# Kernel tuning notes

Measured on AMD Instinct MI355X. Metric: run time of the kernel, lower is better.

Reference implementation:

```python
import jax, jax.numpy as jnp
from jax import lax
import numpy as np
import math

D_MODEL = 1024
D_STATE = 16
DT_RANK = 64  # ceil(1024/16)


def setup_inputs() -> dict:
    key = jax.random.key(0)
    ks = jax.random.split(key, 8)
    B, L = 2, 2048
    x = jax.random.normal(ks[0], (B, L, D_MODEL), dtype=jnp.float32)
    A_log = jnp.full((D_MODEL, D_STATE), math.log(0.5), dtype=jnp.float32)
    x_proj_w = jax.random.normal(ks[1], (DT_RANK + 2 * D_STATE, D_MODEL), dtype=jnp.float32) * (D_MODEL ** -0.5)
    dt_init_std = DT_RANK ** -0.5
    dt_proj_w = jax.random.uniform(ks[2], (D_MODEL, DT_RANK), minval=-dt_init_std, maxval=dt_init_std, dtype=jnp.float32)
    # dt bias init: softplus-inverse of dt sampled log-uniform in [2*dt_min, 2*dt_max] (trend)
    dt = jnp.exp(jax.random.uniform(ks[3], (D_MODEL,), dtype=jnp.float32) * (math.log(0.2) - math.log(0.002)) + math.log(0.002))
    dt = jnp.clip(dt, 1e-4)
    dt_proj_b = dt + jnp.log(-jnp.expm1(-dt))
    D_param = jnp.ones((D_MODEL,), dtype=jnp.float32)
    trend_emphasis = jnp.full((D_MODEL,), 0.1, dtype=jnp.float32)
    return {
        "x": x, "A_log": A_log, "x_proj_w": x_proj_w,
        "dt_proj_w": dt_proj_w, "dt_proj_b": dt_proj_b,
        "D_param": D_param, "trend_emphasis": trend_emphasis,
    }


def _selective_scan(u, delta, A, Bp, Cp, D_param):
    # u, delta: [B,L,D]; A: [D,N]; Bp, Cp: [B,L,N]; D_param: [D]
    deltaA = jnp.exp(jnp.einsum('bld,dn->bldn', delta, A))       # [B,L,D,N]
    deltaBu = jnp.einsum('bld,bln->bldn', delta * u, Bp)          # [B,L,D,N]
    Bsz, L, Dm, N = deltaA.shape

    def step(h, inp):
        dA, dBu, c = inp          # dA,dBu: [B,D,N]; c: [B,N]
        h = dA * h + dBu
        y = jnp.einsum('bdn,bn->bd', h, c)
        return h, y

    h0 = jnp.zeros((Bsz, Dm, N), dtype=u.dtype)
    xs = (jnp.moveaxis(deltaA, 1, 0), jnp.moveaxis(deltaBu, 1, 0), jnp.moveaxis(Cp, 1, 0))
    _, ys = lax.scan(step, h0, xs)            # ys: [L,B,D]
    y = jnp.moveaxis(ys, 0, 1)                # [B,L,D]
    return y + u * D_param


def reference(x, A_log, x_proj_w, dt_proj_w, dt_proj_b, D_param, trend_emphasis):
    # trend component: channel-wise emphasis gate (dropout in eval mode = identity)
    x = x * jax.nn.sigmoid(trend_emphasis)
    xz = x @ x_proj_w.T                                  # [B,L,dt_rank+2N]
    delta_part = xz[..., :DT_RANK]
    Bp = xz[..., DT_RANK:DT_RANK + D_STATE]              # [B,L,N]
    Cp = xz[..., DT_RANK + D_STATE:]                     # [B,L,N]
    delta = jax.nn.softplus(delta_part @ dt_proj_w.T + dt_proj_b)  # [B,L,D]
    A = -jnp.exp(A_log.astype(jnp.float32))
    return _selective_scan(x, delta, A, Bp, Cp, D_param.astype(jnp.float32))
```

## Files before the change

### kernel.cpp

```cpp
#include <hip/hip_runtime.h>
#include <math.h>


#define LOG2E 1.44269504088896340736f
typedef float v2f __attribute__((ext_vector_type(2)));

__device__ __forceinline__ float fexp2(float v){
#if defined(__has_builtin)
#if __has_builtin(__builtin_amdgcn_exp2f)
  return __builtin_amdgcn_exp2f(v);
#else
  return exp2f(v);
#endif
#else
  return exp2f(v);
#endif
}

__device__ __forceinline__ float fsoftplus(float v){
  return fmaxf(v, 0.f) + __logf(1.f + __expf(-fabsf(v)));
}

__global__ __launch_bounds__(256) void k_prep(const float* __restrict__ xpw,
                                              const float* __restrict__ dtw,
                                              const float* __restrict__ alog,
                                              const float* __restrict__ te,
                                              float* __restrict__ w2T,
                                              float* __restrict__ dtwT,
                                              float* __restrict__ A2,
                                              float* __restrict__ sg){
  __shared__ float sm[32 * 33];
  const int bid = blockIdx.x, t = threadIdx.x;
  const int lane = t & 31, srow = t >> 5;
  if (bid < 96){
    const int kt = bid / 3, ct = bid - kt * 3;
#pragma unroll
    for (int r = 0; r < 4; r++){
      const int cr = srow * 4 + r;
      sm[cr * 33 + lane] = xpw[(size_t)(ct * 32 + cr) * 1024 + kt * 32 + lane];
    }
    __syncthreads();
#pragma unroll
    for (int r = 0; r < 4; r++){
      const int kr = srow * 4 + r;
      const int kg = kt * 32 + kr;
      const float s = 1.f / (1.f + __expf(-te[kg]));
      w2T[(size_t)kg * 96 + ct * 32 + lane] = sm[lane * 33 + kr] * s;
    }
  } else if (bid < 160){
    const int idx = bid - 96, dti = idx >> 1, kt2 = idx & 1;
#pragma unroll
    for (int r = 0; r < 4; r++){
      const int cr = srow * 4 + r;
      sm[cr * 33 + lane] = dtw[(size_t)(dti * 32 + cr) * 64 + kt2 * 32 + lane];
    }
    __syncthreads();
#pragma unroll
    for (int r = 0; r < 4; r++){
      const int kr = srow * 4 + r;
      dtwT[(size_t)(kt2 * 32 + kr) * 1024 + dti * 32 + lane] = sm[lane * 33 + kr];
    }
  } else if (bid < 176){
    const int j = (bid - 160) * 1024 + t;
#pragma unroll
    for (int i = 0; i < 4; i++)
      A2[j + i * 256] = -__expf(alog[j + i * 256]) * LOG2E;
  } else {
#pragma unroll
    for (int i = 0; i < 4; i++){
      const int m = i * 256 + t;
      sg[m] = 1.f / (1.f + __expf(-te[m]));
    }
  }
}

__global__ __launch_bounds__(256) void k_xz(const float* __restrict__ x,
                                            const float* __restrict__ w2T,
                                            float* __restrict__ xzp){
  __shared__ float xT[32 * 257];
  const int t = threadIdx.x;
  const int row0 = blockIdx.x * 256;
  const int c0 = blockIdx.y * 32;
  const int kbase = blockIdx.z * 64;
  v2f acc[16];
#pragma unroll
  for (int c = 0; c < 16; c++) acc[c] = (v2f){0.f, 0.f};
  const int kq = t & 7, rsub = t >> 3;
  for (int kt = 0; kt < 2; ++kt){
    const int k0 = kbase + kt * 32;
    __syncthreads();
#pragma unroll
    for (int p = 0; p < 8; p++){
      const int r = p * 32 + rsub;
      const float4 v = *reinterpret_cast<const float4*>(&x[(size_t)(row0 + r) * 1024 + k0 + kq * 4]);
      xT[(kq * 4 + 0) * 257 + r] = v.x;
      xT[(kq * 4 + 1) * 257 + r] = v.y;
      xT[(kq * 4 + 2) * 257 + r] = v.z;
      xT[(kq * 4 + 3) * 257 + r] = v.w;
    }
    __syncthreads();
#pragma unroll 4
    for (int kk = 0; kk < 32; ++kk){
      const float xv = xT[kk * 257 + t];
      const v2f xv2 = {xv, xv};
      const v2f* wr = reinterpret_cast<const v2f*>(&w2T[(size_t)(k0 + kk) * 96 + c0]);
#pragma unroll
      for (int c = 0; c < 16; c++) acc[c] = acc[c] + xv2 * wr[c];
    }
  }
  float4* o = reinterpret_cast<float4*>(xzp + ((size_t)blockIdx.z * 4096 + row0 + t) * 96 + c0);
  const float4* av = reinterpret_cast<const float4*>(acc);
#pragma unroll
  for (int q = 0; q < 8; q++) o[q] = av[q];
}

__global__ __launch_bounds__(256) void k_reduce(const float4* __restrict__ p,
                                                float4* __restrict__ xz){
  const int i = blockIdx.x * 256 + threadIdx.x;
  float4 r = p[i];
#pragma unroll
  for (int s = 1; s < 16; s++){
    const float4 a = p[(size_t)s * 98304 + i];
    r.x += a.x; r.y += a.y; r.z += a.z; r.w += a.w;
  }
  xz[i] = r;
}

__global__ __launch_bounds__(256) void k_scan1(const float* __restrict__ x,
                                               const float* __restrict__ xz,
                                               const float* __restrict__ dtwT,
                                               const float* __restrict__ dtb,
                                               const float* __restrict__ A2,
                                               const float* __restrict__ sg,
                                               float* __restrict__ S,
                                               float* __restrict__ P){
  const int t = threadIdx.x;
  const int chunk = blockIdx.x, dgrp = blockIdx.y, b = blockIdx.z;
  const int d = dgrp * 256 + t;
  const int l0 = chunk * 16;
  v2f wv[32];
#pragma unroll
  for (int k2 = 0; k2 < 32; k2++){
    wv[k2].x = dtwT[(size_t)(2 * k2) * 1024 + d];
    wv[k2].y = dtwT[(size_t)(2 * k2 + 1) * 1024 + d];
  }
  float a2[16];
  {
    const float4* ap = reinterpret_cast<const float4*>(A2 + (size_t)d * 16);
#pragma unroll
    for (int q = 0; q < 4; q++){
      const float4 v = ap[q];
      a2[q*4] = v.x; a2[q*4+1] = v.y; a2[q*4+2] = v.z; a2[q*4+3] = v.w;
    }
  }
  bool uni = true;
#pragma unroll
  for (int n = 1; n < 16; n++) uni = uni && (a2[n] == a2[0]);
  const float sgv = sg[d], dtbv = dtb[d];
  const float* xzb = xz + (size_t)(b * 2048 + l0) * 96;
  float dl[16];
#pragma unroll
  for (int li = 0; li < 16; ++li){
    v2f acc = {dtbv, 0.f};
    const v2f* dp = reinterpret_cast<const v2f*>(xzb + li * 96);
#pragma unroll
    for (int k2 = 0; k2 < 32; k2++) acc = acc + dp[k2] * wv[k2];
    dl[li] = fsoftplus(acc.x + acc.y);
  }
  const size_t xidx = (size_t)(b * 2048 + l0) * 1024 + d;
  const size_t base = ((size_t)((b * 128 + chunk) * 1024 + d)) * 16;
  if (uni){
    const float a2u = a2[0];
    v2f h2[8];
#pragma unroll
    for (int q = 0; q < 8; q++) h2[q] = (v2f){0.f, 0.f};
    float sumd = 0.f;
#pragma unroll 4
    for (int li = 0; li < 16; ++li){
      const float dv = dl[li];
      sumd += dv;
      const float xv = x[xidx + (size_t)li * 1024];
      const float du = dv * xv * sgv;
      const float tt = fexp2(dv * a2u);
      const v2f tt2 = {tt, tt}, du2 = {du, du};
      const v2f* brow = reinterpret_cast<const v2f*>(xzb + li * 96 + 64);
#pragma unroll
      for (int q = 0; q < 8; q++) h2[q] = h2[q] * tt2 + brow[q] * du2;
    }
    const float Ppu = fexp2(a2u * sumd);
    const float4* hv = reinterpret_cast<const float4*>(h2);
#pragma unroll
    for (int q = 0; q < 4; q++)
      *reinterpret_cast<float4*>(&S[base + q * 4]) = hv[q];
    const float4 pv = {Ppu, Ppu, Ppu, Ppu};
#pragma unroll
    for (int q = 0; q < 4; q++)
      *reinterpret_cast<float4*>(&P[base + q * 4]) = pv;
  } else {
    float h[16], Pp[16];
#pragma unroll
    for (int n = 0; n < 16; n++){ h[n] = 0.f; Pp[n] = 1.f; }
    for (int li = 0; li < 16; ++li){
      const float dv = dl[li];
      const float xv = x[xidx + (size_t)li * 1024];
      const float du = dv * xv * sgv;
      const float* brow = xzb + li * 96 + 64;
#pragma unroll
      for (int n = 0; n < 16; n++){
        const float tt = fexp2(dv * a2[n]);
        h[n] = fmaf(tt, h[n], du * brow[n]);
        Pp[n] *= tt;
      }
    }
#pragma unroll
    for (int q = 0; q < 4; q++){
      float4 v; v.x = h[q*4]; v.y = h[q*4+1]; v.z = h[q*4+2]; v.w = h[q*4+3];
      *reinterpret_cast<float4*>(&S[base + q * 4]) = v;
      float4 u; u.x = Pp[q*4]; u.y = Pp[q*4+1]; u.z = Pp[q*4+2]; u.w = Pp[q*4+3];
      *reinterpret_cast<float4*>(&P[base + q * 4]) = u;
    }
  }
}

__global__ __launch_bounds__(128) void k_scan2(const float* __restrict__ S,
                                               const float* __restrict__ P,
                                               float* __restrict__ H){
  const int g = blockIdx.x * 128 + threadIdx.x;
  const int n = g & 15, dd = (g >> 4) & 1023, bb = g >> 14;
  float h = 0.f;
#pragma unroll 8
  for (int c = 0; c < 128; c++){
    const size_t idx = ((size_t)((bb * 128 + c) * 1024 + dd)) * 16 + n;
    H[idx] = h;
    h = fmaf(P[idx], h, S[idx]);
  }
}

__global__ __launch_bounds__(256) void k_scan3(const float* __restrict__ x,
                                               const float* __restrict__ xz,
                                               const float* __restrict__ dtwT,
                                               const float* __restrict__ dtb,
                                               const float* __restrict__ A2,
                                               const float* __restrict__ sg,
                                               const float* __restrict__ Dpar,
                                               const float* __restrict__ H,
                                               float* __restrict__ out){
  const int t = threadIdx.x;
  const int chunk = blockIdx.x, dgrp = blockIdx.y, b = blockIdx.z;
  const int d = dgrp * 256 + t;
  const int l0 = chunk * 16;
  v2f wv[32];
#pragma unroll
  for (int k2 = 0; k2 < 32; k2++){
    wv[k2].x = dtwT[(size_t)(2 * k2) * 1024 + d];
    wv[k2].y = dtwT[(size_t)(2 * k2 + 1) * 1024 + d];
  }
  float a2[16];
  {
    const float4* ap = reinterpret_cast<const float4*>(A2 + (size_t)d * 16);
#pragma unroll
    for (int q = 0; q < 4; q++){
      const float4 v = ap[q];
      a2[q*4] = v.x; a2[q*4+1] = v.y; a2[q*4+2] = v.z; a2[q*4+3] = v.w;
    }
  }
  bool uni = true;
#pragma unroll
  for (int n = 1; n < 16; n++) uni = uni && (a2[n] == a2[0]);
  const float sgv = sg[d], dtbv = dtb[d], Dv = Dpar[d];
  const float* xzb = xz + (size_t)(b * 2048 + l0) * 96;
  float dl[16];
#pragma unroll
  for (int li = 0; li < 16; ++li){
    v2f acc = {dtbv, 0.f};
    const v2f* dp = reinterpret_cast<const v2f*>(xzb + li * 96);
#pragma unroll
    for (int k2 = 0; k2 < 32; k2++) acc = acc + dp[k2] * wv[k2];
    dl[li] = fsoftplus(acc.x + acc.y);
  }
  const size_t xidx = (size_t)(b * 2048 + l0) * 1024 + d;
  const size_t hbase = ((size_t)((b * 128 + chunk) * 1024 + d)) * 16;
  if (uni){
    const float a2u = a2[0];
    v2f h2[8];
    {
      const float4* hp = reinterpret_cast<const float4*>(H + hbase);
      float4* hd = reinterpret_cast<float4*>(h2);
#pragma unroll
      for (int q = 0; q < 4; q++) hd[q] = hp[q];
    }
#pragma unroll 4
    for (int li = 0; li < 16; ++li){
      const float dv = dl[li];
      const float xv = x[xidx + (size_t)li * 1024];
      const float du = dv * xv * sgv;
      const float tt = fexp2(dv * a2u);
      const v2f tt2 = {tt, tt}, du2 = {du, du};
      const v2f* brow = reinterpret_cast<const v2f*>(xzb + li * 96 + 64);
      const v2f* crow = reinterpret_cast<const v2f*>(xzb + li * 96 + 80);
      v2f yv = {0.f, 0.f};
#pragma unroll
      for (int q = 0; q < 8; q++){
        h2[q] = h2[q] * tt2 + brow[q] * du2;
        yv = yv + h2[q] * crow[q];
      }
      out[xidx + (size_t)li * 1024] = fmaf(xv * sgv, Dv, yv.x + yv.y);
    }
  } else {
    float h[16];
    {
      const float4* hp = reinterpret_cast<const float4*>(H + hbase);
#pragma unroll
      for (int q = 0; q < 4; q++){
        const float4 v = hp[q];
        h[q*4] = v.x; h[q*4+1] = v.y; h[q*4+2] = v.z; h[q*4+3] = v.w;
      }
    }
    for (int li = 0; li < 16; ++li){
      const float dv = dl[li];
      const float xv = x[xidx + (size_t)li * 1024];
      const float du = dv * xv * sgv;
      const float* brow = xzb + li * 96 + 64;
      float y = 0.f;
#pragma unroll
      for (int n = 0; n < 16; n++){
        const float tt = fexp2(dv * a2[n]);
        h[n] = fmaf(tt, h[n], du * brow[n]);
        y = fmaf(h[n], brow[16 + n], y);
      }
      out[xidx + (size_t)li * 1024] = fmaf(xv * sgv, Dv, y);
    }
  }
}

extern "C" void kernel_launch(void* const* d_in, const int* in_sizes, int n_in,
                              void* d_out, int out_size, void* d_ws, size_t ws_size,
                              hipStream_t stream){
  const float* x    = (const float*)d_in[0];
  const float* Alog = (const float*)d_in[1];
  const float* xpw  = (const float*)d_in[2];
  const float* dtw  = (const float*)d_in[3];
  const float* dtb  = (const float*)d_in[4];
  const float* Dpar = (const float*)d_in[5];
  const float* te   = (const float*)d_in[6];
  float* out = (float*)d_out;
  char* ws = (char*)d_ws;

  float* w2T  = (float*)(ws);
  float* A2   = (float*)(ws + 393216);
  float* sg   = (float*)(ws + 458752);
  float* dtwT = (float*)(ws + 462848);
  float* xz   = (float*)(ws + 724992);
  float* xzp  = (float*)(ws + 2297856);
  float* S    = (float*)(ws + 27463680);
  float* P    = (float*)(ws + 44240896);
  float* Hst  = (float*)(ws + 61018112);

  hipLaunchKernelGGL(k_prep,   dim3(177),        dim3(256), 0, stream, xpw, dtw, Alog, te, w2T, dtwT, A2, sg);
  hipLaunchKernelGGL(k_xz,     dim3(16, 3, 16),  dim3(256), 0, stream, x, w2T, xzp);
  hipLaunchKernelGGL(k_reduce, dim3(384),        dim3(256), 0, stream, (const float4*)xzp, (float4*)xz);
  hipLaunchKernelGGL(k_scan1,  dim3(128, 4, 2),  dim3(256), 0, stream, x, xz, dtwT, dtb, A2, sg, S, P);
  hipLaunchKernelGGL(k_scan2,  dim3(256),        dim3(128), 0, stream, S, P, Hst);
  hipLaunchKernelGGL(k_scan3,  dim3(128, 4, 2),  dim3(256), 0, stream, x, xz, dtwT, dtb, A2, sg, Dpar, Hst, out);
}
```

Measured before the change: 163.7 us.

## Precompute delta once in separate kernel and parallelize inter-chunk scan across segments

Adds a k_delta kernel that computes softplus(dt projection) once into a workspace buffer, so scan1 and scan3 no longer each repeat the 64-wide dot product and dtw register loads. Rewrites k_scan2 to split the 128 chunks into 8 segments per block, combine them through shared memory, then apply the carries. Scan2 now runs 1024 blocks instead of 256 to expose more parallelism. The cost is an extra 16MB delta buffer write and two reads, plus an additional kernel launch.

```diff
diff --git a/kernel.cpp b/kernel.cpp
--- a/kernel.cpp
+++ b/kernel.cpp
@@ -126,10 +126,34 @@
   xz[i] = r;
 }
 
-__global__ __launch_bounds__(256) void k_scan1(const float* __restrict__ x,
-                                               const float* __restrict__ xz,
+__global__ __launch_bounds__(256) void k_delta(const float* __restrict__ xz,
                                                const float* __restrict__ dtwT,
                                                const float* __restrict__ dtb,
+                                               float* __restrict__ del){
+  const int t = threadIdx.x;
+  const int r0 = blockIdx.x * 16;
+  const int d = blockIdx.y * 256 + t;
+  v2f wv[32];
+#pragma unroll
+  for (int k2 = 0; k2 < 32; k2++){
+    wv[k2].x = dtwT[(size_t)(2 * k2) * 1024 + d];
+    wv[k2].y = dtwT[(size_t)(2 * k2 + 1) * 1024 + d];
+  }
+  const float dtbv = dtb[d];
+  const float* xzb = xz + (size_t)r0 * 96;
+#pragma unroll 4
+  for (int li = 0; li < 16; ++li){
+    v2f acc = {dtbv, 0.f};
+    const v2f* dp = reinterpret_cast<const v2f*>(xzb + li * 96);
+#pragma unroll
+    for (int k2 = 0; k2 < 32; k2++) acc = acc + dp[k2] * wv[k2];
+    del[(size_t)(r0 + li) * 1024 + d] = fsoftplus(acc.x + acc.y);
+  }
+}
+
+__global__ __launch_bounds__(256) void k_scan1(const float* __restrict__ x,
+                                               const float* __restrict__ del,
+                                               const float* __restrict__ xz,
                                                const float* __restrict__ A2,
                                                const float* __restrict__ sg,
                                                float* __restrict__ S,
@@ -138,12 +162,6 @@
   const int chunk = blockIdx.x, dgrp = blockIdx.y, b = blockIdx.z;
   const int d = dgrp * 256 + t;
   const int l0 = chunk * 16;
-  v2f wv[32];
-#pragma unroll
-  for (int k2 = 0; k2 < 32; k2++){
-    wv[k2].x = dtwT[(size_t)(2 * k2) * 1024 + d];
-    wv[k2].y = dtwT[(size_t)(2 * k2 + 1) * 1024 + d];
-  }
   float a2[16];
   {
     const float4* ap = reinterpret_cast<const float4*>(A2 + (size_t)d * 16);
@@ -156,18 +174,15 @@
   bool uni = true;
 #pragma unroll
   for (int n = 1; n < 16; n++) uni = uni && (a2[n] == a2[0]);
-  const float sgv = sg[d], dtbv = dtb[d];
+  const float sgv = sg[d];
+  const size_t xidx = (size_t)(b * 2048 + l0) * 1024 + d;
+  float dl[16], du[16];
+#pragma unroll
+  for (int li = 0; li < 16; ++li){
+    dl[li] = del[xidx + (size_t)li * 1024];
+    du[li] = dl[li] * x[xidx + (size_t)li * 1024] * sgv;
+  }
   const float* xzb = xz + (size_t)(b * 2048 + l0) * 96;
-  float dl[16];
-#pragma unroll
-  for (int li = 0; li < 16; ++li){
-    v2f acc = {dtbv, 0.f};
-    const v2f* dp = reinterpret_cast<const v2f*>(xzb + li * 96);
-#pragma unroll
-    for (int k2 = 0; k2 < 32; k2++) acc = acc + dp[k2] * wv[k2];
-    dl[li] = fsoftplus(acc.x + acc.y);
-  }
-  const size_t xidx = (size_t)(b * 2048 + l0) * 1024 + d;
   const size_t base = ((size_t)((b * 128 + chunk) * 1024 + d)) * 16;
   if (uni){
     const float a2u = a2[0];
@@ -177,17 +192,14 @@
     float sumd = 0.f;
 #pragma unroll 4
     for (int li = 0; li < 16; ++li){
-      const float dv = dl[li];
-      sumd += dv;
-      const float xv = x[xidx + (size_t)li * 1024];
-      const float du = dv * xv * sgv;
-      const float tt = fexp2(dv * a2u);
-      const v2f tt2 = {tt, tt}, du2 = {du, du};
+      sumd += dl[li];
+      const float tt = fexp2(dl[li] * a2u);
+      const v2f tt2 = {tt, tt}, du2 = {du[li], du[li]};
       const v2f* brow = reinterpret_cast<const v2f*>(xzb + li * 96 + 64);
 #pragma unroll
       for (int q = 0; q < 8; q++) h2[q] = h2[q] * tt2 + brow[q] * du2;
     }
-    const float Ppu = fexp2(a2u * sumd);
+    const float Ppu = fexp2(a2[0] * sumd);
     const float4* hv = reinterpret_cast<const float4*>(h2);
 #pragma unroll
     for (int q = 0; q < 4; q++)
@@ -201,14 +213,11 @@
 #pragma unroll
     for (int n = 0; n < 16; n++){ h[n] = 0.f; Pp[n] = 1.f; }
     for (int li = 0; li < 16; ++li){
-      const float dv = dl[li];
-      const float xv = x[xidx + (size_t)li * 1024];
-      const float du = dv * xv * sgv;
       const float* brow = xzb + li * 96 + 64;
 #pragma unroll
       for (int n = 0; n < 16; n++){
-        const float tt = fexp2(dv * a2[n]);
-        h[n] = fmaf(tt, h[n], du * brow[n]);
+        const float tt = fexp2(dl[li] * a2[n]);
+        h[n] = fmaf(tt, h[n], du[li] * brow[n]);
         Pp[n] *= tt;
       }
     }
@@ -222,24 +231,41 @@
   }
 }
 
-__global__ __launch_bounds__(128) void k_scan2(const float* __restrict__ S,
+__global__ __launch_bounds__(256) void k_scan2(const float* __restrict__ S,
                                                const float* __restrict__ P,
                                                float* __restrict__ H){
-  const int g = blockIdx.x * 128 + threadIdx.x;
-  const int n = g & 15, dd = (g >> 4) & 1023, bb = g >> 14;
+  __shared__ float ls[256], lp[256];
+  const int t = threadIdx.x;
+  const int dn = t & 31, seg = t >> 5;
+  const int n = dn & 15, dloc = dn >> 4;
+  const int bid = blockIdx.x;
+  const int b = bid >> 9, dpair = bid & 511;
+  const int d = dpair * 2 + dloc;
+  const size_t sbase = ((size_t)(b * 128) * 1024 + d) * 16 + n;
+  float s = 0.f, p = 1.f;
+#pragma unroll 4
+  for (int i = 0; i < 16; i++){
+    const size_t idx = sbase + (size_t)(seg * 16 + i) * 16384;
+    const float Sv = S[idx], Pv = P[idx];
+    s = fmaf(Pv, s, Sv);
+    p *= Pv;
+  }
+  ls[t] = s; lp[t] = p;
+  __syncthreads();
   float h = 0.f;
-#pragma unroll 8
-  for (int c = 0; c < 128; c++){
-    const size_t idx = ((size_t)((bb * 128 + c) * 1024 + dd)) * 16 + n;
+  for (int j = 0; j < seg; j++)
+    h = fmaf(lp[j * 32 + dn], h, ls[j * 32 + dn]);
+#pragma unroll 4
+  for (int i = 0; i < 16; i++){
+    const size_t idx = sbase + (size_t)(seg * 16 + i) * 16384;
     H[idx] = h;
     h = fmaf(P[idx], h, S[idx]);
   }
 }
 
 __global__ __launch_bounds__(256) void k_scan3(const float* __restrict__ x,
+                                               const float* __restrict__ del,
                                                const float* __restrict__ xz,
-                                               const float* __restrict__ dtwT,
-                                               const float* __restrict__ dtb,
                                                const float* __restrict__ A2,
                                                const float* __restrict__ sg,
                                                const float* __restrict__ Dpar,
@@ -249,12 +275,6 @@
   const int chunk = blockIdx.x, dgrp = blockIdx.y, b = blockIdx.z;
   const int d = dgrp * 256 + t;
   const int l0 = chunk * 16;
-  v2f wv[32];
-#pragma unroll
-  for (int k2 = 0; k2 < 32; k2++){
-    wv[k2].x = dtwT[(size_t)(2 * k2) * 1024 + d];
-    wv[k2].y = dtwT[(size_t)(2 * k2 + 1) * 1024 + d];
-  }
   float a2[16];
   {
     const float4* ap = reinterpret_cast<const float4*>(A2 + (size_t)d * 16);
@@ -267,18 +287,16 @@
   bool uni = true;
 #pragma unroll
   for (int n = 1; n < 16; n++) uni = uni && (a2[n] == a2[0]);
-  const float sgv = sg[d], dtbv = dtb[d], Dv = Dpar[d];
+  const float sgv = sg[d], Dv = Dpar[d];
+  const size_t xidx = (size_t)(b * 2048 + l0) * 1024 + d;
+  float dl[16], du[16], xd[16];
+#pragma unroll
+  for (int li = 0; li < 16; ++li){
+    dl[li] = del[xidx + (size_t)li * 1024];
+    xd[li] = x[xidx + (size_t)li * 1024] * sgv;
+    du[li] = dl[li] * xd[li];
+  }
   const float* xzb = xz + (size_t)(b * 2048 + l0) * 96;
-  float dl[16];
-#pragma unroll
-  for (int li = 0; li < 16; ++li){
-    v2f acc = {dtbv, 0.f};
-    const v2f* dp = reinterpret_cast<const v2f*>(xzb + li * 96);
-#pragma unroll
-    for (int k2 = 0; k2 < 32; k2++) acc = acc + dp[k2] * wv[k2];
-    dl[li] = fsoftplus(acc.x + acc.y);
-  }
-  const size_t xidx = (size_t)(b * 2048 + l0) * 1024 + d;
   const size_t hbase = ((size_t)((b * 128 + chunk) * 1024 + d)) * 16;
   if (uni){
     const float a2u = a2[0];
@@ -291,11 +309,8 @@
     }
 #pragma unroll 4
     for (int li = 0; li < 16; ++li){
-      const float dv = dl[li];
-      const float xv = x[xidx + (size_t)li * 1024];
-      const float du = dv * xv * sgv;
-      const float tt = fexp2(dv * a2u);
-      const v2f tt2 = {tt, tt}, du2 = {du, du};
+      const float tt = fexp2(dl[li] * a2u);
+      const v2f tt2 = {tt, tt}, du2 = {du[li], du[li]};
       const v2f* brow = reinterpret_cast<const v2f*>(xzb + li * 96 + 64);
       const v2f* crow = reinterpret_cast<const v2f*>(xzb + li * 96 + 80);
       v2f yv = {0.f, 0.f};
@@ -304,7 +319,7 @@
         h2[q] = h2[q] * tt2 + brow[q] * du2;
         yv = yv + h2[q] * crow[q];
       }
-      out[xidx + (size_t)li * 1024] = fmaf(xv * sgv, Dv, yv.x + yv.y);
+      out[xidx + (size_t)li * 1024] = fmaf(xd[li], Dv, yv.x + yv.y);
     }
   } else {
     float h[16];
@@ -317,18 +332,15 @@
       }
     }
     for (int li = 0; li < 16; ++li){
-      const float dv = dl[li];
-      const float xv = x[xidx + (size_t)li * 1024];
-      const float du = dv * xv * sgv;
       const float* brow = xzb + li * 96 + 64;
       float y = 0.f;
 #pragma unroll
       for (int n = 0; n < 16; n++){
-        const float tt = fexp2(dv * a2[n]);
-        h[n] = fmaf(tt, h[n], du * brow[n]);
+        const float tt = fexp2(dl[li] * a2[n]);
+        h[n] = fmaf(tt, h[n], du[li] * brow[n]);
         y = fmaf(h[n], brow[16 + n], y);
       }
-      out[xidx + (size_t)li * 1024] = fmaf(xv * sgv, Dv, y);
+      out[xidx + (size_t)li * 1024] = fmaf(xd[li], Dv, y);
     }
   }
 }
@@ -351,15 +363,17 @@
   float* sg   = (float*)(ws + 458752);
   float* dtwT = (float*)(ws + 462848);
   float* xz   = (float*)(ws + 724992);
-  float* xzp  = (float*)(ws + 2297856);
-  float* S    = (float*)(ws + 27463680);
-  float* P    = (float*)(ws + 44240896);
-  float* Hst  = (float*)(ws + 61018112);
+  float* del  = (float*)(ws + 2297856);
+  float* xzp  = (float*)(ws + 19075072);
+  float* S    = (float*)(ws + 44240896);
+  float* P    = (float*)(ws + 61018112);
+  float* Hst  = (float*)(ws + 77795328);
 
   hipLaunchKernelGGL(k_prep,   dim3(177),        dim3(256), 0, stream, xpw, dtw, Alog, te, w2T, dtwT, A2, sg);
   hipLaunchKernelGGL(k_xz,     dim3(16, 3, 16),  dim3(256), 0, stream, x, w2T, xzp);
   hipLaunchKernelGGL(k_reduce, dim3(384),        dim3(256), 0, stream, (const float4*)xzp, (float4*)xz);
-  hipLaunchKernelGGL(k_scan1,  dim3(128, 4, 2),  dim3(256), 0, stream, x, xz, dtwT, dtb, A2, sg, S, P);
-  hipLaunchKernelGGL(k_scan2,  dim3(256),        dim3(128), 0, stream, S, P, Hst);
-  hipLaunchKernelGGL(k_scan3,  dim3(128, 4, 2),  dim3(256), 0, stream, x, xz, dtwT, dtb, A2, sg, Dpar, Hst, out);
-}
+  hipLaunchKernelGGL(k_delta,  dim3(256, 4),     dim3(256), 0, stream, xz, dtwT, dtb, del);
+  hipLaunchKernelGGL(k_scan1,  dim3(128, 4, 2),  dim3(256), 0, stream, x, del, xz, A2, sg, S, P);
+  hipLaunchKernelGGL(k_scan2,  dim3(1024),       dim3(256), 0, stream, S, P, Hst);
+  hipLaunchKernelGGL(k_scan3,  dim3(128, 4, 2),  dim3(256), 0, stream, x, del, xz, A2, sg, Dpar, Hst, out);
+}
```

Result: no change. 163.0 us (-0.5%).
